# Kernel tuning notes

Measured on AMD Instinct MI355X. Metric: run time of the kernel, lower is better.

Reference implementation:

```python
import jax, jax.numpy as jnp
import numpy as np

SAMPLE_RATE = 48000
FREQ_MIN, FREQ_MAX = 20.0, 2000.0
MOD_MIN, MOD_MAX = -1.0, 2.0


def setup_inputs() -> dict:
    key = jax.random.key(0)
    k1, k2, k3 = jax.random.split(key, 3)
    B, N = 512, 65536
    freq = jax.random.uniform(k1, (B, 1), dtype=jnp.float32)
    mod_env = jax.random.uniform(k2, (B, N), dtype=jnp.float32)
    mod_amount = jax.random.uniform(k3, (B, 1), dtype=jnp.float32)
    return {"num_samples": N, "freq": freq, "mod_env": mod_env, "mod_amount": mod_amount}


def reference(num_samples, freq, mod_env, mod_amount):
    # de-normalize controls
    f0 = FREQ_MIN + (FREQ_MAX - FREQ_MIN) * freq            # [B, 1] Hz
    f0 = 2.0 * jnp.pi * f0 / SAMPLE_RATE                    # [B, 1] rad/sample
    mod_amt = MOD_MIN + (MOD_MAX - MOD_MIN) * mod_amount    # [B, 1]
    # instantaneous angular frequency per sample: f0 * (1 + mod_env * mod_amt)
    freq_env = f0 + mod_env * mod_amt * f0                  # [B, N]
    # prepend zero, cumsum, drop last -> exclusive prefix sum (phase)
    padded = jnp.concatenate([jnp.zeros_like(freq_env[:, :1]), freq_env], axis=-1)
    phase = jnp.cumsum(padded, axis=-1)[:, :-1]             # [B, N]
    return jnp.sin(phase)
```

## Files before the change

kernel.cpp:

```cpp
#include <hip/hip_runtime.h>


constexpr int BLOCK = 1024;
constexpr int VPT   = 8;
constexpr int NW    = BLOCK / 64;

typedef float f32x4 __attribute__((ext_vector_type(4)));

__global__ __launch_bounds__(BLOCK) void osc_kernel(
    const float* __restrict__ freq,
    const float* __restrict__ mod_env,
    const float* __restrict__ mod_amount,
    float* __restrict__ out,
    int N)
{
    const int row  = blockIdx.x;
    const int tid  = threadIdx.x;
    const int lane = tid & 63;
    const int wid  = tid >> 6;

    __shared__ double s_wsum[2][NW];

    const double f0rev = (20.0 + 1980.0 * (double)freq[row]) / 48000.0;
    const double amt   = -1.0 + 3.0 * (double)mod_amount[row];
    const double k     = f0rev * amt;

    const float* __restrict__ rowp = mod_env + (size_t)row * N;
    float* __restrict__ outp       = out     + (size_t)row * N;

    const int chunk  = BLOCK * VPT;
    const int nchunk = N / chunk;

    double carry = 0.0;

    const float* p0 = rowp + tid * VPT;
    f32x4 curA = *(const f32x4*)(p0);
    f32x4 curB = *(const f32x4*)(p0 + 4);

    for (int c = 0; c < nchunk; ++c) {
        f32x4 nxtA = curA, nxtB = curB;
        if (c + 1 < nchunk) {
            const float* p = rowp + (size_t)(c + 1) * chunk + tid * VPT;
            nxtA = *(const f32x4*)(p);
            nxtB = *(const f32x4*)(p + 4);
        }

        double v0 = fma((double)curA.x, k, f0rev);
        double v1 = fma((double)curA.y, k, f0rev);
        double v2 = fma((double)curA.z, k, f0rev);
        double v3 = fma((double)curA.w, k, f0rev);
        double v4 = fma((double)curB.x, k, f0rev);
        double v5 = fma((double)curB.y, k, f0rev);
        double v6 = fma((double)curB.z, k, f0rev);
        double v7 = fma((double)curB.w, k, f0rev);

        double tsum = ((v0 + v1) + (v2 + v3)) + ((v4 + v5) + (v6 + v7));

        double x = tsum;
        #pragma unroll
        for (int off = 1; off < 64; off <<= 1) {
            double y = __shfl_up(x, off, 64);
            if (lane >= off) x += y;
        }

        if (lane == 63) s_wsum[c & 1][wid] = x;
        __syncthreads();

        double w = (lane < NW) ? s_wsum[c & 1][lane] : 0.0;
        #pragma unroll
        for (int off = 1; off < NW; off <<= 1) {
            double y = __shfl_up(w, off, 64);
            if (lane >= off) w += y;
        }
        double total = __shfl(w, NW - 1, 64);
        double exc   = __shfl(w, (wid > 0 ? wid - 1 : 0), 64);
        if (wid == 0) exc = 0.0;

        double phase = carry + exc + (x - tsum);
        carry += total;

        f32x4 oA, oB;
        {
            double pf;
            pf = phase - floor(phase); oA.x = __builtin_amdgcn_sinf((float)pf); phase += v0;
            pf = phase - floor(phase); oA.y = __builtin_amdgcn_sinf((float)pf); phase += v1;
            pf = phase - floor(phase); oA.z = __builtin_amdgcn_sinf((float)pf); phase += v2;
            pf = phase - floor(phase); oA.w = __builtin_amdgcn_sinf((float)pf); phase += v3;
            pf = phase - floor(phase); oB.x = __builtin_amdgcn_sinf((float)pf); phase += v4;
            pf = phase - floor(phase); oB.y = __builtin_amdgcn_sinf((float)pf); phase += v5;
            pf = phase - floor(phase); oB.z = __builtin_amdgcn_sinf((float)pf); phase += v6;
            pf = phase - floor(phase); oB.w = __builtin_amdgcn_sinf((float)pf); phase += v7;
        }

        float* q = outp + (size_t)c * chunk + tid * VPT;
        __builtin_nontemporal_store(oA, (f32x4*)(q));
        __builtin_nontemporal_store(oB, (f32x4*)(q + 4));

        curA = nxtA; curB = nxtB;
    }
}

extern "C" void kernel_launch(void* const* d_in, const int* in_sizes, int n_in,
                              void* d_out, int out_size, void* d_ws, size_t ws_size,
                              hipStream_t stream) {
    const float* freq       = (const float*)d_in[1];
    const float* mod_env    = (const float*)d_in[2];
    const float* mod_amount = (const float*)d_in[3];
    float* out = (float*)d_out;

    const int B = in_sizes[1];
    const int N = in_sizes[2] / B;

    osc_kernel<<<B, BLOCK, 0, stream>>>(freq, mod_env, mod_amount, out, N);
}
```

Measured before the change: 56.04 us.

## Compute per-thread local phase in fp32 and double elements per thread

Moves the per-element frequency computation and the in-thread running prefix from double to float, keeping double only for the cross-thread scan and carry. It doubles elements per thread to 16, which halves the number of block scans and barriers per row. Nontemporal stores become plain stores. This cuts the FP64 work that is slow relative to FP32, at the cost of some phase accuracy within each thread's run and higher register pressure.

```diff
diff --git a/kernel.cpp b/kernel.cpp
--- a/kernel.cpp
+++ b/kernel.cpp
@@ -2,7 +2,7 @@
 
 
 constexpr int BLOCK = 1024;
-constexpr int VPT   = 8;
+constexpr int VPT   = 16;
 constexpr int NW    = BLOCK / 64;
 
 typedef float f32x4 __attribute__((ext_vector_type(4)));
@@ -23,7 +23,9 @@
 
     const double f0rev = (20.0 + 1980.0 * (double)freq[row]) / 48000.0;
     const double amt   = -1.0 + 3.0 * (double)mod_amount[row];
-    const double k     = f0rev * amt;
+    const double kd    = f0rev * amt;
+    const float  kf    = (float)kd;
+    const float  f0f   = (float)f0rev;
 
     const float* __restrict__ rowp = mod_env + (size_t)row * N;
     float* __restrict__ outp       = out     + (size_t)row * N;
@@ -33,29 +35,39 @@
 
     double carry = 0.0;
 
-    const float* p0 = rowp + tid * VPT;
-    f32x4 curA = *(const f32x4*)(p0);
-    f32x4 curB = *(const f32x4*)(p0 + 4);
+    f32x4 cur0, cur1, cur2, cur3;
+    {
+        const float* p = rowp + tid * VPT;
+        cur0 = *(const f32x4*)(p);
+        cur1 = *(const f32x4*)(p + 4);
+        cur2 = *(const f32x4*)(p + 8);
+        cur3 = *(const f32x4*)(p + 12);
+    }
 
     for (int c = 0; c < nchunk; ++c) {
-        f32x4 nxtA = curA, nxtB = curB;
+        f32x4 nxt0 = cur0, nxt1 = cur1, nxt2 = cur2, nxt3 = cur3;
         if (c + 1 < nchunk) {
             const float* p = rowp + (size_t)(c + 1) * chunk + tid * VPT;
-            nxtA = *(const f32x4*)(p);
-            nxtB = *(const f32x4*)(p + 4);
+            nxt0 = *(const f32x4*)(p);
+            nxt1 = *(const f32x4*)(p + 4);
+            nxt2 = *(const f32x4*)(p + 8);
+            nxt3 = *(const f32x4*)(p + 12);
         }
 
-        double v0 = fma((double)curA.x, k, f0rev);
-        double v1 = fma((double)curA.y, k, f0rev);
-        double v2 = fma((double)curA.z, k, f0rev);
-        double v3 = fma((double)curA.w, k, f0rev);
-        double v4 = fma((double)curB.x, k, f0rev);
-        double v5 = fma((double)curB.y, k, f0rev);
-        double v6 = fma((double)curB.z, k, f0rev);
-        double v7 = fma((double)curB.w, k, f0rev);
+        float vv[VPT] = { cur0.x, cur0.y, cur0.z, cur0.w,
+                          cur1.x, cur1.y, cur1.z, cur1.w,
+                          cur2.x, cur2.y, cur2.z, cur2.w,
+                          cur3.x, cur3.y, cur3.z, cur3.w };
+        float lv[VPT];
+        float s = 0.0f;
+        #pragma unroll
+        for (int i = 0; i < VPT; ++i) {
+            float vi = fmaf(vv[i], kf, f0f);
+            lv[i] = s;
+            s += vi;
+        }
 
-        double tsum = ((v0 + v1) + (v2 + v3)) + ((v4 + v5) + (v6 + v7));
-
+        double tsum = (double)s;
         double x = tsum;
         #pragma unroll
         for (int off = 1; off < 64; off <<= 1) {
@@ -79,24 +91,23 @@
         double phase = carry + exc + (x - tsum);
         carry += total;
 
-        f32x4 oA, oB;
-        {
-            double pf;
-            pf = phase - floor(phase); oA.x = __builtin_amdgcn_sinf((float)pf); phase += v0;
-            pf = phase - floor(phase); oA.y = __builtin_amdgcn_sinf((float)pf); phase += v1;
-            pf = phase - floor(phase); oA.z = __builtin_amdgcn_sinf((float)pf); phase += v2;
-            pf = phase - floor(phase); oA.w = __builtin_amdgcn_sinf((float)pf); phase += v3;
-            pf = phase - floor(phase); oB.x = __builtin_amdgcn_sinf((float)pf); phase += v4;
-            pf = phase - floor(phase); oB.y = __builtin_amdgcn_sinf((float)pf); phase += v5;
-            pf = phase - floor(phase); oB.z = __builtin_amdgcn_sinf((float)pf); phase += v6;
-            pf = phase - floor(phase); oB.w = __builtin_amdgcn_sinf((float)pf); phase += v7;
+        float bf = (float)(phase - floor(phase));
+
+        float o[VPT];
+        #pragma unroll
+        for (int i = 0; i < VPT; ++i) {
+            float pf = bf + lv[i];
+            pf = pf - floorf(pf);
+            o[i] = __builtin_amdgcn_sinf(pf);
         }
 
         float* q = outp + (size_t)c * chunk + tid * VPT;
-        __builtin_nontemporal_store(oA, (f32x4*)(q));
-        __builtin_nontemporal_store(oB, (f32x4*)(q + 4));
+        *(f32x4*)(q)      = (f32x4){ o[0],  o[1],  o[2],  o[3]  };
+        *(f32x4*)(q + 4)  = (f32x4){ o[4],  o[5],  o[6],  o[7]  };
+        *(f32x4*)(q + 8)  = (f32x4){ o[8],  o[9],  o[10], o[11] };
+        *(f32x4*)(q + 12) = (f32x4){ o[12], o[13], o[14], o[15] };
 
-        curA = nxtA; curB = nxtB;
+        cur0 = nxt0; cur1 = nxt1; cur2 = nxt2; cur3 = nxt3;
     }
 }
 
```

Result: no change. 56.08 us (+0.1%).

## Use fp32 per-element phase math and wave-contiguous float4 layout

Applied to the files above, without the earlier changes.

Moves the per-element frequency FMA, local sums and phase accumulation from double to float, keeping only the cross-lane scan and carry in double. Changes the data layout so each wave handles two contiguous 256-float segments with float4 per lane, giving fully coalesced 16-byte accesses instead of 32-byte per-thread strides. This requires a two-component wave scan. It also swaps the nontemporal stores for plain stores. The goal is to cut the cost of slow fp64 ALU work, at the risk of small extra phase error from fp32 accumulation within each segment.

```diff
diff --git a/kernel.cpp b/kernel.cpp
--- a/kernel.cpp
+++ b/kernel.cpp
@@ -4,6 +4,7 @@
 constexpr int BLOCK = 1024;
 constexpr int VPT   = 8;
 constexpr int NW    = BLOCK / 64;
+constexpr int WELEM = 64 * VPT;
 
 typedef float f32x4 __attribute__((ext_vector_type(4)));
 
@@ -23,47 +24,46 @@
 
     const double f0rev = (20.0 + 1980.0 * (double)freq[row]) / 48000.0;
     const double amt   = -1.0 + 3.0 * (double)mod_amount[row];
-    const double k     = f0rev * amt;
-
-    const float* __restrict__ rowp = mod_env + (size_t)row * N;
-    float* __restrict__ outp       = out     + (size_t)row * N;
+    const float  kf    = (float)(f0rev * amt);
+    const float  f0f   = (float)f0rev;
 
     const int chunk  = BLOCK * VPT;
     const int nchunk = N / chunk;
 
+    const float* __restrict__ wload  = mod_env + (size_t)row * N + wid * WELEM + 4 * lane;
+    float*       __restrict__ wstore = out     + (size_t)row * N + wid * WELEM + 4 * lane;
+
     double carry = 0.0;
 
-    const float* p0 = rowp + tid * VPT;
-    f32x4 curA = *(const f32x4*)(p0);
-    f32x4 curB = *(const f32x4*)(p0 + 4);
+    f32x4 curA = *(const f32x4*)(wload);
+    f32x4 curB = *(const f32x4*)(wload + 256);
 
     for (int c = 0; c < nchunk; ++c) {
         f32x4 nxtA = curA, nxtB = curB;
         if (c + 1 < nchunk) {
-            const float* p = rowp + (size_t)(c + 1) * chunk + tid * VPT;
+            const float* p = wload + (size_t)(c + 1) * chunk;
             nxtA = *(const f32x4*)(p);
-            nxtB = *(const f32x4*)(p + 4);
+            nxtB = *(const f32x4*)(p + 256);
         }
 
-        double v0 = fma((double)curA.x, k, f0rev);
-        double v1 = fma((double)curA.y, k, f0rev);
-        double v2 = fma((double)curA.z, k, f0rev);
-        double v3 = fma((double)curA.w, k, f0rev);
-        double v4 = fma((double)curB.x, k, f0rev);
-        double v5 = fma((double)curB.y, k, f0rev);
-        double v6 = fma((double)curB.z, k, f0rev);
-        double v7 = fma((double)curB.w, k, f0rev);
+        float va0 = fmaf(curA.x, kf, f0f), va1 = fmaf(curA.y, kf, f0f);
+        float va2 = fmaf(curA.z, kf, f0f), va3 = fmaf(curA.w, kf, f0f);
+        float vb0 = fmaf(curB.x, kf, f0f), vb1 = fmaf(curB.y, kf, f0f);
+        float vb2 = fmaf(curB.z, kf, f0f), vb3 = fmaf(curB.w, kf, f0f);
 
-        double tsum = ((v0 + v1) + (v2 + v3)) + ((v4 + v5) + (v6 + v7));
+        float sa = (va0 + va1) + (va2 + va3);
+        float sb = (vb0 + vb1) + (vb2 + vb3);
 
-        double x = tsum;
+        double xa = (double)sa, xb = (double)sb;
         #pragma unroll
         for (int off = 1; off < 64; off <<= 1) {
-            double y = __shfl_up(x, off, 64);
-            if (lane >= off) x += y;
+            double ya = __shfl_up(xa, off, 64);
+            double yb = __shfl_up(xb, off, 64);
+            if (lane >= off) { xa += ya; xb += yb; }
         }
+        double Ta = __shfl(xa, 63, 64);
 
-        if (lane == 63) s_wsum[c & 1][wid] = x;
+        if (lane == 63) s_wsum[c & 1][wid] = xa + xb;
         __syncthreads();
 
         double w = (lane < NW) ? s_wsum[c & 1][lane] : 0.0;
@@ -76,25 +76,33 @@
         double exc   = __shfl(w, (wid > 0 ? wid - 1 : 0), 64);
         if (wid == 0) exc = 0.0;
 
-        double phase = carry + exc + (x - tsum);
+        double base = carry + exc;
         carry += total;
+
+        double ph0 = base + (xa - (double)sa);
+        double ph1 = base + Ta + (xb - (double)sb);
+
+        float bf0 = (float)(ph0 - floor(ph0));
+        float bf1 = (float)(ph1 - floor(ph1));
 
         f32x4 oA, oB;
         {
-            double pf;
-            pf = phase - floor(phase); oA.x = __builtin_amdgcn_sinf((float)pf); phase += v0;
-            pf = phase - floor(phase); oA.y = __builtin_amdgcn_sinf((float)pf); phase += v1;
-            pf = phase - floor(phase); oA.z = __builtin_amdgcn_sinf((float)pf); phase += v2;
-            pf = phase - floor(phase); oA.w = __builtin_amdgcn_sinf((float)pf); phase += v3;
-            pf = phase - floor(phase); oB.x = __builtin_amdgcn_sinf((float)pf); phase += v4;
-            pf = phase - floor(phase); oB.y = __builtin_amdgcn_sinf((float)pf); phase += v5;
-            pf = phase - floor(phase); oB.z = __builtin_amdgcn_sinf((float)pf); phase += v6;
-            pf = phase - floor(phase); oB.w = __builtin_amdgcn_sinf((float)pf); phase += v7;
+            float pf, fr;
+            pf = bf0;
+            fr = pf - floorf(pf); oA.x = __builtin_amdgcn_sinf(fr); pf += va0;
+            fr = pf - floorf(pf); oA.y = __builtin_amdgcn_sinf(fr); pf += va1;
+            fr = pf - floorf(pf); oA.z = __builtin_amdgcn_sinf(fr); pf += va2;
+            fr = pf - floorf(pf); oA.w = __builtin_amdgcn_sinf(fr);
+            pf = bf1;
+            fr = pf - floorf(pf); oB.x = __builtin_amdgcn_sinf(fr); pf += vb0;
+            fr = pf - floorf(pf); oB.y = __builtin_amdgcn_sinf(fr); pf += vb1;
+            fr = pf - floorf(pf); oB.z = __builtin_amdgcn_sinf(fr); pf += vb2;
+            fr = pf - floorf(pf); oB.w = __builtin_amdgcn_sinf(fr);
         }
 
-        float* q = outp + (size_t)c * chunk + tid * VPT;
-        __builtin_nontemporal_store(oA, (f32x4*)(q));
-        __builtin_nontemporal_store(oB, (f32x4*)(q + 4));
+        float* q = wstore + (size_t)c * chunk;
+        *(f32x4*)(q)       = oA;
+        *(f32x4*)(q + 256) = oB;
 
         curA = nxtA; curB = nxtB;
     }
```

Measured after the change: 46.08 us. -17.8%, faster.
